# Kernel optimization log

Hardware: AMD Instinct MI355X
Metric: run time of the kernel (lower is better)

## Reference

```python
import jax, jax.numpy as jnp
import numpy as np

B, L, H, V = 64, 8, 4096, 50257


def setup_inputs() -> dict:
    key = jax.random.key(0)
    ks = jax.random.split(key, 5)
    return {
        "embedding": jax.random.normal(ks[0], (V, H), jnp.float32) * 0.02,
        "hidden_states": jax.random.normal(ks[1], (B, L, H), jnp.float32),
        "output_position": 7,  # scalar index of the position to sample from
        "temperatures": jax.random.uniform(ks[2], (B,), jnp.float32, 0.5, 1.5),
        "top_ps": jax.random.uniform(ks[3], (B,), jnp.float32, 0.7, 1.0),
        "tops_ks": jax.random.randint(ks[4], (B,), 1, 64),  # top-k in [1,64)
        "embedding_bias": jnp.zeros((V,), jnp.float32),
    }


def reference(embedding, hidden_states, output_position, temperatures, top_ps, tops_ks, embedding_bias):
    # select the output position: [B, H]
    h = hidden_states[:, output_position, :]
    # logits GEMM against tied embedding: [B, V]
    logits = jnp.einsum("bh,vh->bv", h, embedding) + embedding_bias[None, :]
    logits = logits / temperatures[:, None]
    probs = jax.nn.softmax(logits.astype(jnp.float32), axis=-1)

    # descending sort of probabilities
    order = jnp.argsort(-probs, axis=-1)                       # [B, V]
    probs_sort = jnp.take_along_axis(probs, order, axis=-1)    # [B, V]

    # top-p mask: exclusive cumulative sum exceeding top_p
    cum = jnp.cumsum(probs_sort, axis=-1)
    topp_mask = (cum - probs_sort) > top_ps[:, None]
    # top-k mask: rank >= k
    ranks = jnp.arange(V, dtype=tops_ks.dtype)[None, :]
    topk_mask = ranks >= tops_ks[:, None]

    probs_sort = jnp.where(topp_mask | topk_mask, 0.0, probs_sort)
    probs_sort = probs_sort / jnp.sum(probs_sort, axis=-1, keepdims=True)

    # scatter back to original vocab order via inverse permutation
    inv = jnp.argsort(order, axis=-1)
    probs_final = jnp.take_along_axis(probs_sort, inv, axis=-1)  # [B, V]

    # multinomial sampling (1 sample per row)
    logp = jnp.where(probs_final > 0, jnp.log(jnp.maximum(probs_final, 1e-38)), -jnp.inf)
    next_token_ids = jax.random.categorical(jax.random.key(42), logp, axis=-1)
    return next_token_ids
```

## Files before the change

### kernel.cpp

```cpp
#include <hip/hip_runtime.h>
#include <stdint.h>
#include <float.h>
#include <limits.h>


typedef __bf16 bf16x8 __attribute__((ext_vector_type(8)));
typedef float  f32x4  __attribute__((ext_vector_type(4)));

__device__ __forceinline__ void split8v(const float* f, bf16x8& hi, bf16x8& lo) {
#pragma unroll
    for (int e = 0; e < 8; ++e) {
        const __bf16 h = (__bf16)f[e];
        hi[e] = h;
        lo[e] = (__bf16)(f[e] - (float)h);
    }
}
__device__ __forceinline__ void split8(const float* f, uint4& hi, uint4& lo) {
    bf16x8 vh, vl;
    split8v(f, vh, vl);
    hi = __builtin_bit_cast(uint4, vh);
    lo = __builtin_bit_cast(uint4, vl);
}

__global__ __launch_bounds__(256) void prep_h(
    const float* __restrict__ hs, const int* __restrict__ pos_p,
    unsigned short* __restrict__ Ahi, unsigned short* __restrict__ Alo,
    int H, int L)
{
    const int pos = pos_p[0];
    const int tid = blockIdx.x * 256 + threadIdx.x;
    const int b     = tid >> 8;
    const int kbase = (tid & 255) * 16;
    const float* src = hs + ((size_t)b * L + pos) * H + kbase;
    float f[16];
    *(float4*)&f[0]  = *(const float4*)(src);
    *(float4*)&f[4]  = *(const float4*)(src + 4);
    *(float4*)&f[8]  = *(const float4*)(src + 8);
    *(float4*)&f[12] = *(const float4*)(src + 12);

    const int r16 = b >> 4, ll = b & 15;
    const int kc  = kbase >> 5;
    const int lh0 = (kbase >> 3) & 3;
#pragma unroll
    for (int c = 0; c < 2; ++c) {
        uint4 hi, lo;
        split8(f + 8 * c, hi, lo);
        const size_t dst = ((size_t)(r16 * 128 + kc) * 64 + (lh0 + c) * 16 + ll) * 8;
        *(uint4*)&Ahi[dst] = hi;
        *(uint4*)&Alo[dst] = lo;
    }
}

__global__ __launch_bounds__(256, 2) void logits_mfma(
    const float* __restrict__ emb,
    const unsigned short* __restrict__ Ahi,
    const unsigned short* __restrict__ Alo,
    const float* __restrict__ temps,
    const float* __restrict__ bias,
    float*       __restrict__ out,
    int V, int H)
{
    __shared__ float sB[4 * 4096];

    const int tid  = threadIdx.x;
    const int lane = tid & 63;
    const int w    = tid >> 6;
    const int v0   = blockIdx.x * 64;

    const int ll = lane & 15;
    const int lh = lane >> 4;
    const int lrow = lane >> 5;
    const int lcol = lane & 31;

    const int NT = H >> 5;
    const int NH = H >> 7;

    float* swave = &sB[w * 4096];

    const size_t aoff = (size_t)lh * 128 + (size_t)ll * 8;

    bf16x8 aih[2][4], ail[2][4];
    float4 fB[4][2];
    f32x4  acc[4];
#pragma unroll
    for (int i = 0; i < 4; ++i) acc[i] = (f32x4){0.f, 0.f, 0.f, 0.f};

#define STAGE(hw, hb) do {                                                    \
    _Pragma("unroll")                                                         \
    for (int i = 0; i < 16; i += 2) {                                         \
        const int ri = i + lrow;                                              \
        int rg = v0 + w * 16 + ri;                                            \
        rg = (rg < V) ? rg : (V - 1);                                         \
        const float* srcp = emb + (size_t)rg * H + (hw) * 128                 \
                          + ((lcol * 4) ^ ((ri & 7) << 2));                   \
        __builtin_amdgcn_global_load_lds(                                     \
            (const __attribute__((address_space(1))) void*)srcp,              \
            (__attribute__((address_space(3))) void*)&swave[(hb) * 2048 + i * 128], \
            16, 0, 0);                                                        \
    }                                                                         \
} while (0)

#define DSREAD(hb) do {                                                       \
    _Pragma("unroll")                                                         \
    for (int kt = 0; kt < 4; ++kt) {                                          \
        _Pragma("unroll")                                                     \
        for (int q = 0; q < 2; ++q) {                                         \
            const int fi = (kt * 32 + lh * 8 + q * 4) ^ ((ll & 7) << 2);      \
            fB[kt][q] = *(const float4*)&swave[(hb) * 2048 + ll * 128 + fi];  \
        }                                                                     \
    }                                                                         \
} while (0)

#define LOADA(t, p) do {                                                      \
    _Pragma("unroll")                                                         \
    for (int i = 0; i < 4; ++i) {                                             \
        const size_t ai = aoff + (size_t)i * 65536 + (size_t)(t) * 512;       \
        aih[p][i] = *(const bf16x8*)&Ahi[ai];                                 \
        ail[p][i] = *(const bf16x8*)&Alo[ai];                                 \
    }                                                                         \
} while (0)

    LOADA(0, 0);
    STAGE(0, 0);

    for (int hw = 0; hw < NH; ++hw) {
        const int hb = hw & 1;
        DSREAD(hb);
        if (hw + 1 < NH) STAGE(hw + 1, hb ^ 1);

#pragma unroll
        for (int kt = 0; kt < 4; ++kt) {
            const int t = hw * 4 + kt;
            if (t + 1 < NT) LOADA(t + 1, (kt + 1) & 1);

            float f[8];
            *(float4*)&f[0] = fB[kt][0];
            *(float4*)&f[4] = fB[kt][1];
            bf16x8 fbh, fbl;
            split8v(f, fbh, fbl);

#pragma unroll
            for (int i = 0; i < 4; ++i) {
                acc[i] = __builtin_amdgcn_mfma_f32_16x16x32_bf16(
                    ail[kt & 1][i], fbh, acc[i], 0, 0, 0);
                acc[i] = __builtin_amdgcn_mfma_f32_16x16x32_bf16(
                    aih[kt & 1][i], fbl, acc[i], 0, 0, 0);
                acc[i] = __builtin_amdgcn_mfma_f32_16x16x32_bf16(
                    aih[kt & 1][i], fbh, acc[i], 0, 0, 0);
            }
        }
    }
#undef STAGE
#undef DSREAD
#undef LOADA

    const int vv = v0 + 16 * w + ll;
    if (vv < V) {
        const float bv = bias[vv];
#pragma unroll
        for (int i = 0; i < 4; ++i)
#pragma unroll
            for (int r = 0; r < 4; ++r) {
                const int b = 16 * i + lh * 4 + r;
                out[(size_t)b * V + vv] = (acc[i][r] + bv) / temps[b];
            }
    }
}

__device__ __forceinline__ uint32_t rotl32(uint32_t x, int d) {
    return (x << d) | (x >> (32 - d));
}

__device__ float jax_gumbel(uint32_t flat) {
    const uint32_t k0 = 0u, k1 = 42u;
    const uint32_t ks[3] = { k0, k1, k0 ^ k1 ^ 0x1BD11BDAu };
    uint32_t x0 = 0u   + ks[0];
    uint32_t x1 = flat + ks[1];
    const int rot[2][4] = { {13, 15, 26, 6}, {17, 29, 16, 24} };
#pragma unroll
    for (int r = 0; r < 5; ++r) {
        const int* rr = rot[r & 1];
#pragma unroll
        for (int j = 0; j < 4; ++j) {
            x0 += x1;
            x1 = rotl32(x1, rr[j]);
            x1 ^= x0;
        }
        x0 += ks[(r + 1) % 3];
        x1 += ks[(r + 2) % 3] + (uint32_t)(r + 1);
    }
    const uint32_t bits = x0 ^ x1;
    const uint32_t fb = (bits >> 9) | 0x3F800000u;
    const float f = __uint_as_float(fb) - 1.0f;
    const float tiny = 1.17549435e-38f;
    float u = __fadd_rn(__fmul_rn(f, 1.0f), tiny);
    u = fmaxf(tiny, u);
    const float l1 = logf(u);
    return -logf(-l1);
}

#define NBINS 4096
#define CAP   2048
#define NKEEP 64

__global__ __launch_bounds__(256) void sample_kernel(
    const float* __restrict__ logits,
    const float* __restrict__ top_ps,
    const int*   __restrict__ top_ks,
    int*         __restrict__ out_ids,
    int V)
{
    const int b = blockIdx.x;
    const int tid = threadIdx.x;
    const float* row = logits + (size_t)b * V;

    __shared__ float swred[4];
    __shared__ int   bins[NBINS];
    __shared__ int   schunk[256];
    __shared__ int   sThrBin, sCnt, sMkeep;
    __shared__ float cval[CAP];
    __shared__ int   cidx[CAP];
    __shared__ float tval[NKEEP];
    __shared__ int   tidxs[NKEEP];

    float m = -INFINITY;
    for (int k = tid; k < V; k += 256) m = fmaxf(m, row[k]);
#pragma unroll
    for (int o = 32; o > 0; o >>= 1) m = fmaxf(m, __shfl_xor(m, o, 64));
    if ((tid & 63) == 0) swred[tid >> 6] = m;
    __syncthreads();
    m = fmaxf(fmaxf(swred[0], swred[1]), fmaxf(swred[2], swred[3]));

    for (int k = tid; k < NBINS; k += 256) bins[k] = 0;
    if (tid == 0) sCnt = 0;
    __syncthreads();

    float s = 0.f;
    for (int k = tid; k < V; k += 256) {
        const float x = row[k];
        s += expf(x - m);
        const float g = m - x;
        int bin = (int)(g * 256.0f);
        if (bin >= NBINS) bin = NBINS - 1;
        atomicAdd(&bins[bin], 1);
    }
#pragma unroll
    for (int o = 32; o > 0; o >>= 1) s += __shfl_xor(s, o, 64);
    __syncthreads();
    if ((tid & 63) == 0) swred[tid >> 6] = s;

    int csum = 0;
#pragma unroll
    for (int k = 0; k < NBINS / 256; ++k) csum += bins[tid * (NBINS / 256) + k];
    schunk[tid] = csum;
    __syncthreads();
    s = swred[0] + swred[1] + swred[2] + swred[3];
    if (tid == 0) {
        int cum = 0, chunk = 255;
        for (int c = 0; c < 256; ++c) {
            if (cum + schunk[c] >= NKEEP) { chunk = c; break; }
            cum += schunk[c];
        }
        int t = NBINS - 1;
        const int base = chunk * (NBINS / 256);
        for (int k = base; k < base + NBINS / 256; ++k) {
            cum += bins[k];
            if (cum >= NKEEP) { t = k; break; }
        }
        sThrBin = t;
    }
    __syncthreads();
    const int thrBin = sThrBin;

    for (int k = tid; k < V; k += 256) {
        const float x = row[k];
        const float g = m - x;
        int bin = (int)(g * 256.0f);
        if (bin >= NBINS) bin = NBINS - 1;
        if (bin <= thrBin) {
            const int p = atomicAdd(&sCnt, 1);
            if (p < CAP) { cval[p] = x; cidx[p] = k; }
        }
    }
    __syncthreads();
    const int C = min(sCnt, CAP);

    for (int i = tid; i < C; i += 256) {
        const float vi = cval[i];
        const int   ii = cidx[i];
        int rank = 0;
        for (int j = 0; j < C; ++j) {
            const float vj = cval[j];
            const int   ij = cidx[j];
            rank += (vj > vi) || (vj == vi && ij < ii);
        }
        if (rank < NKEEP) { tval[rank] = vi; tidxs[rank] = ii; }
    }
    __syncthreads();

    if (tid == 0) {
        const float pb = top_ps[b];
        const int   kk = top_ks[b];
        const int   nk = min(NKEEP, C);
        float cum = 0.f;
        int mk = 0;
        for (int r = 0; r < nk; ++r) {
            const float pr = expf(tval[r] - m) / s;
            cum += pr;
            const float excl = cum - pr;
            if (excl > pb || r >= kk) break;
            ++mk;
        }
        sMkeep = (mk > 0) ? mk : 1;
    }
    __syncthreads();
    const int mkeep = sMkeep;

    if (tid < 64) {
        float sc = -INFINITY;
        int vid = INT_MAX;
        if (tid < mkeep) {
            const int v = tidxs[tid];
            vid = v;
            sc = tval[tid] + jax_gumbel((uint32_t)b * (uint32_t)V + (uint32_t)v);
        }
#pragma unroll
        for (int o = 32; o > 0; o >>= 1) {
            const float os = __shfl_xor(sc, o, 64);
            const int   ov = __shfl_xor(vid, o, 64);
            if (os > sc || (os == sc && ov < vid)) { sc = os; vid = ov; }
        }
        if (tid == 0) out_ids[b] = vid;
    }
}

extern "C" void kernel_launch(void* const* d_in, const int* in_sizes, int n_in,
                              void* d_out, int out_size, void* d_ws, size_t ws_size,
                              hipStream_t stream)
{
    const float* emb   = (const float*)d_in[0];
    const float* hs    = (const float*)d_in[1];
    const int*   pos   = (const int*)d_in[2];
    const float* temps = (const float*)d_in[3];
    const float* tps   = (const float*)d_in[4];
    const int*   tks   = (const int*)d_in[5];
    const float* bias  = (const float*)d_in[6];

    const int B = in_sizes[3];
    const int V = in_sizes[6];
    const int H = (int)((long long)in_sizes[0] / V);
    const int L = (int)((long long)in_sizes[1] / ((long long)B * H));

    float*          logits = (float*)d_ws;
    unsigned short* Ahi    = (unsigned short*)((char*)d_ws + (16u << 20));
    unsigned short* Alo    = Ahi + (size_t)B * H;

    prep_h<<<(B * H) / (16 * 256), 256, 0, stream>>>(hs, pos, Ahi, Alo, H, L);

    const int nblk = (V + 63) / 64;
    logits_mfma<<<nblk, 256, 0, stream>>>(emb, Ahi, Alo, temps, bias,
                                          logits, V, H);

    sample_kernel<<<B, 256, 0, stream>>>(logits, tps, tks, (int*)d_out, V);
}
```

Baseline: 399.8 us.

## Split logits GEMM by batch across waves with shared 16-row vocab tiles

The logits kernel now gives each block 16 vocab rows instead of 64. Its four waves split the 64 batch rows, and all of them read a shared, block-wide double-buffered LDS window of 512 K-elements, synchronised with __syncthreads. Blocks also start at staggered K windows to spread memory traffic. This raises the block count about fourfold for better occupancy and load balance. The cost is that each wave now streams the hi and lo A fragments over the full K range with less register reuse, and a block barrier is added per window.

```diff
diff --git a/kernel.cpp b/kernel.cpp
--- a/kernel.cpp
+++ b/kernel.cpp
@@ -45,11 +45,14 @@
     for (int c = 0; c < 2; ++c) {
         uint4 hi, lo;
         split8(f + 8 * c, hi, lo);
-        const size_t dst = ((size_t)(r16 * 128 + kc) * 64 + (lh0 + c) * 16 + ll) * 8;
+        const size_t dst = ((size_t)(r16 * (H >> 5) + kc) * 64 + (lh0 + c) * 16 + ll) * 8;
         *(uint4*)&Ahi[dst] = hi;
         *(uint4*)&Alo[dst] = lo;
     }
 }
+
+#define NWF    512
+#define WTILES 16
 
 __global__ __launch_bounds__(256, 2) void logits_mfma(
     const float* __restrict__ emb,
@@ -60,110 +63,93 @@
     float*       __restrict__ out,
     int V, int H)
 {
-    __shared__ float sB[4 * 4096];
+    __shared__ float sB[2][16 * NWF];
 
     const int tid  = threadIdx.x;
     const int lane = tid & 63;
     const int w    = tid >> 6;
-    const int v0   = blockIdx.x * 64;
+    const int v0   = blockIdx.x * 16;
 
     const int ll = lane & 15;
     const int lh = lane >> 4;
-    const int lrow = lane >> 5;
-    const int lcol = lane & 31;
-
-    const int NT = H >> 5;
-    const int NH = H >> 7;
-
-    float* swave = &sB[w * 4096];
-
-    const size_t aoff = (size_t)lh * 128 + (size_t)ll * 8;
-
-    bf16x8 aih[2][4], ail[2][4];
-    float4 fB[4][2];
-    f32x4  acc[4];
-#pragma unroll
-    for (int i = 0; i < 4; ++i) acc[i] = (f32x4){0.f, 0.f, 0.f, 0.f};
-
-#define STAGE(hw, hb) do {                                                    \
+
+    const int NWIN = H / NWF;
+    const int NTT  = H >> 5;
+    const int wst  = (blockIdx.x & 3) * 2;
+
+    const size_t aoff = (size_t)w * ((size_t)H * 16)
+                      + (size_t)lh * 128 + (size_t)ll * 8;
+
+    bf16x8 aih[2], ail[2];
+    f32x4  acc = (f32x4){0.f, 0.f, 0.f, 0.f};
+
+#define STAGE(win, bf) do {                                                   \
     _Pragma("unroll")                                                         \
-    for (int i = 0; i < 16; i += 2) {                                         \
-        const int ri = i + lrow;                                              \
-        int rg = v0 + w * 16 + ri;                                            \
+    for (int rr = 0; rr < 4; ++rr) {                                          \
+        const int r = w * 4 + rr;                                             \
+        int rg = v0 + r;                                                      \
         rg = (rg < V) ? rg : (V - 1);                                         \
-        const float* srcp = emb + (size_t)rg * H + (hw) * 128                 \
-                          + ((lcol * 4) ^ ((ri & 7) << 2));                   \
-        __builtin_amdgcn_global_load_lds(                                     \
-            (const __attribute__((address_space(1))) void*)srcp,              \
-            (__attribute__((address_space(3))) void*)&swave[(hb) * 2048 + i * 128], \
-            16, 0, 0);                                                        \
-    }                                                                         \
-} while (0)
-
-#define DSREAD(hb) do {                                                       \
-    _Pragma("unroll")                                                         \
-    for (int kt = 0; kt < 4; ++kt) {                                          \
+        const float* rowp = emb + (size_t)rg * H + (size_t)(win) * NWF        \
+                          + ((lane * 4) ^ ((r & 15) << 2));                   \
         _Pragma("unroll")                                                     \
-        for (int q = 0; q < 2; ++q) {                                         \
-            const int fi = (kt * 32 + lh * 8 + q * 4) ^ ((ll & 7) << 2);      \
-            fB[kt][q] = *(const float4*)&swave[(hb) * 2048 + ll * 128 + fi];  \
+        for (int c = 0; c < 2; ++c) {                                         \
+            __builtin_amdgcn_global_load_lds(                                 \
+                (const __attribute__((address_space(1))) void*)(rowp + c * 256), \
+                (__attribute__((address_space(3))) void*)&sB[bf][r * NWF + c * 256], \
+                16, 0, 0);                                                    \
         }                                                                     \
     }                                                                         \
 } while (0)
 
-#define LOADA(t, p) do {                                                      \
-    _Pragma("unroll")                                                         \
-    for (int i = 0; i < 4; ++i) {                                             \
-        const size_t ai = aoff + (size_t)i * 65536 + (size_t)(t) * 512;       \
-        aih[p][i] = *(const bf16x8*)&Ahi[ai];                                 \
-        ail[p][i] = *(const bf16x8*)&Alo[ai];                                 \
-    }                                                                         \
+#define LOADA(T, p) do {                                                      \
+    const size_t ai = aoff + (size_t)(T) * 512;                               \
+    aih[p] = *(const bf16x8*)&Ahi[ai];                                        \
+    ail[p] = *(const bf16x8*)&Alo[ai];                                        \
 } while (0)
 
-    LOADA(0, 0);
-    STAGE(0, 0);
-
-    for (int hw = 0; hw < NH; ++hw) {
-        const int hb = hw & 1;
-        DSREAD(hb);
-        if (hw + 1 < NH) STAGE(hw + 1, hb ^ 1);
-
-#pragma unroll
-        for (int kt = 0; kt < 4; ++kt) {
-            const int t = hw * 4 + kt;
-            if (t + 1 < NT) LOADA(t + 1, (kt + 1) & 1);
-
+    LOADA(wst * WTILES, 0);
+    STAGE(wst, 0);
+    __syncthreads();
+
+    for (int ws = 0; ws < NWIN; ++ws) {
+        const int bf = ws & 1;
+        if (ws + 1 < NWIN) STAGE((wst + ws + 1) & (NWIN - 1), bf ^ 1);
+
+#pragma unroll
+        for (int kt = 0; kt < WTILES; ++kt) {
+            const int p = kt & 1;
+            if (!(ws == NWIN - 1 && kt == WTILES - 1)) {
+                const int wsn = ws + ((kt + 1) >> 4);
+                const int ktn = (kt + 1) & 15;
+                const int T1  = (((wst + wsn) & (NWIN - 1)) << 4) + ktn;
+                LOADA(T1, p ^ 1);
+            }
+
+            const int f0   = kt * 32 + lh * 8;
+            const int sidx = ll << 2;
             float f[8];
-            *(float4*)&f[0] = fB[kt][0];
-            *(float4*)&f[4] = fB[kt][1];
+            *(float4*)&f[0] = *(const float4*)&sB[bf][ll * NWF + ((f0)     ^ sidx)];
+            *(float4*)&f[4] = *(const float4*)&sB[bf][ll * NWF + ((f0 + 4) ^ sidx)];
             bf16x8 fbh, fbl;
             split8v(f, fbh, fbl);
 
-#pragma unroll
-            for (int i = 0; i < 4; ++i) {
-                acc[i] = __builtin_amdgcn_mfma_f32_16x16x32_bf16(
-                    ail[kt & 1][i], fbh, acc[i], 0, 0, 0);
-                acc[i] = __builtin_amdgcn_mfma_f32_16x16x32_bf16(
-                    aih[kt & 1][i], fbl, acc[i], 0, 0, 0);
-                acc[i] = __builtin_amdgcn_mfma_f32_16x16x32_bf16(
-                    aih[kt & 1][i], fbh, acc[i], 0, 0, 0);
-            }
-        }
+            acc = __builtin_amdgcn_mfma_f32_16x16x32_bf16(ail[p], fbh, acc, 0, 0, 0);
+            acc = __builtin_amdgcn_mfma_f32_16x16x32_bf16(aih[p], fbl, acc, 0, 0, 0);
+            acc = __builtin_amdgcn_mfma_f32_16x16x32_bf16(aih[p], fbh, acc, 0, 0, 0);
+        }
+        __syncthreads();
     }
 #undef STAGE
-#undef DSREAD
 #undef LOADA
 
-    const int vv = v0 + 16 * w + ll;
+    const int vv = v0 + ll;
     if (vv < V) {
         const float bv = bias[vv];
 #pragma unroll
-        for (int i = 0; i < 4; ++i)
-#pragma unroll
-            for (int r = 0; r < 4; ++r) {
-                const int b = 16 * i + lh * 4 + r;
-                out[(size_t)b * V + vv] = (acc[i][r] + bv) / temps[b];
-            }
+        for (int r = 0; r < 4; ++r) {
+            const int b = w * 16 + lh * 4 + r;
+            out[(size_t)b * V + vv] = (acc[r] + bv) / temps[b];
+        }
     }
 }
 
@@ -357,7 +343,7 @@
 
     prep_h<<<(B * H) / (16 * 256), 256, 0, stream>>>(hs, pos, Ahi, Alo, H, L);
 
-    const int nblk = (V + 63) / 64;
+    const int nblk = (V + 15) / 16;
     logits_mfma<<<nblk, 256, 0, stream>>>(emb, Ahi, Alo, temps, bias,
                                           logits, V, H);
 
```

New measurement: 381.7 us. -4.5%, faster.
